# Optimization experiments

Measured on AMD Instinct MI355X. Metric: run time of the kernel, lower is better.

The kernel has to match this reference:

```python
import jax, jax.numpy as jnp
import numpy as np
from functools import partial

N_SEEDS = 1000       # n
BG_LOW, BG_UP = 0.3, 0.7
ERODE_K, ERODE_ITER = 11, 1
KSZ = 3
IGNORE = -255
INT_MAX = np.iinfo(np.int32).max


def _min_pool2d(x, k):
    # binary erosion with a kxk all-ones structuring element, SAME padding
    return jax.lax.reduce_window(x, INT_MAX, jax.lax.min, (k, k), (1, 1), 'SAME')


def _max_pool3d(x, k):
    # binary dilation over (B,H,W) with kxk window on spatial dims
    return jax.lax.reduce_window(x, -INT_MAX, jax.lax.max, (1, k, k), (1, 1, 1), 'SAME')


def _otsu_threshold(flat255):
    # flat255: int32 pixel values in [0,255]
    hist = jnp.zeros(256, jnp.float32).at[flat255].add(1.0)
    total = jnp.asarray(flat255.shape[0], jnp.float32)
    bins = jnp.arange(256, dtype=jnp.float32)
    w = jnp.cumsum(hist)                 # class-0 pixel count up to bin t
    m = jnp.cumsum(hist * bins)          # class-0 intensity mass up to t
    mT = m[-1]
    denom = w * (total - w)
    sigma_b = jnp.where(denom > 0, (mT * w - total * m) ** 2 / (denom * total * total), 0.0)
    th = jnp.argmax(sigma_b).astype(jnp.float32)
    bad = jnp.sum(hist > 0) <= 1         # degenerate histogram -> bad_egg
    return th, bad


def _sample_mask(eligible, key, hw):
    # uniform sampling without replacement of min(N_SEEDS, #eligible)
    # via random-score top-k restricted to eligible positions
    scores = jnp.where(eligible, jax.random.uniform(key, (hw,)), -jnp.inf)
    vals, idx = jax.lax.top_k(scores, N_SEEDS)
    sel = (vals > -jnp.inf).astype(jnp.int32)
    return jnp.zeros(hw, jnp.int32).at[idx].max(sel)


def _one_sample(cam, key):
    h, w = cam.shape
    hw = h * w
    cam255 = jnp.floor(cam * 255.0)
    flat255 = jnp.clip(cam255.astype(jnp.int32).ravel(), 0, 255)

    th, bad = _otsu_threshold(flat255)
    th = jnp.where(bad, jnp.median(cam * 255.0), th)
    th = jnp.where(th == 0, 1.0, jnp.where(th == 255, 254.0, th))

    roi = (cam255 > th).astype(jnp.int32)
    for _ in range(ERODE_ITER):
        roi = _min_pool2d(roi, ERODE_K)

    kf, kb, kz = jax.random.split(key, 3)
    # foreground: sample uniformly from eroded ROI pixels
    fg = _sample_mask(roi.ravel() == 1, kf, hw)
    # background: sample uniformly from the nbr_bg lowest-activation pixels
    z = jax.random.uniform(kz, (), minval=BG_LOW, maxval=BG_UP)
    nbr_bg = jnp.ceil(z * hw)
    order = jnp.argsort(cam.ravel())
    rank = jnp.zeros(hw, jnp.int32).at[order].set(jnp.arange(hw, dtype=jnp.int32))
    bg = _sample_mask(rank.astype(jnp.float32) < nbr_bg, kb, hw)
    return fg.reshape(h, w), bg.reshape(h, w)


def setup_inputs() -> dict:
    key = jax.random.key(0)
    x = jax.random.uniform(key, (128, 1, 512, 512), dtype=jnp.float32)
    return {"x": x}


def reference(x):
    b, d, h, w = x.shape
    keys = jax.random.split(jax.random.key(42), b)
    all_fg, all_bg = jax.vmap(_one_sample)(x[:, 0], keys)   # (B,H,W) int32
    # dilation with ksz x ksz ones kernel
    all_fg = _max_pool3d(all_fg, KSZ)
    all_bg = _max_pool3d(all_bg, KSZ)
    outer = all_fg + all_bg
    all_fg = jnp.where(outer == 2, 0, all_fg)
    all_bg = jnp.where(outer == 2, 0, all_bg)
    out = jnp.full((b, h, w), IGNORE, dtype=jnp.int32)
    out = jnp.where(all_fg == 1, 1, out)
    out = jnp.where(all_bg == 1, 0, out)
    return out
```

## Files before the change

### kernel.cpp

```cpp
#include <hip/hip_runtime.h>
#include <cstdint>

typedef unsigned short u16;

constexpr int BATCH = 128;
constexpr int H = 512, W = 512;
constexpr int HW = H * W;
constexpr int WPR = W / 64;
constexpr int WPI = HW / 64;
constexpr int NSEED = 1000;
constexpr int MARGIN = 3000;
constexpr int CAP2 = 4096;
constexpr int CAPS = 1024;
constexpr int LBUF = 2048;
constexpr int NBIN = 4096;
constexpr int QSEG = 128;

__device__ __forceinline__ uint32_t rotl32(uint32_t v, int d) {
  return (v << d) | (v >> (32 - d));
}

__device__ __forceinline__ void tf2x32(uint32_t k0, uint32_t k1,
                                       uint32_t x0, uint32_t x1,
                                       uint32_t &o0, uint32_t &o1) {
// ... 121 lines not shown
__global__ __launch_bounds__(256) void k_otsu(const uint32_t* __restrict__ gh,
                                              const uint32_t* __restrict__ kbg,
                                              int* __restrict__ th_out,
                                              uint32_t* __restrict__ b1a,
                                              uint32_t* __restrict__ r1a) {
  __shared__ uint32_t h[NBIN];
  __shared__ float Lc[511], Sc[511], Lm[511], Sm[511];
  __shared__ float av[4];
  __shared__ int ai[4];
  int b = blockIdx.x, t = threadIdx.x;
  const uint32_t* g0 = gh + ((size_t)(b * 4 + 0) << 12);
  const uint32_t* g1 = gh + ((size_t)(b * 4 + 1) << 12);
  const uint32_t* g2 = gh + ((size_t)(b * 4 + 2) << 12);
  const uint32_t* g3 = gh + ((size_t)(b * 4 + 3) << 12);
  for (int i = t; i < NBIN; i += 256) h[i] = g0[i] + g1[i] + g2[i] + g3[i];
  __syncthreads();
  uint32_t hv = 0;
#pragma unroll
  for (int i = 0; i < 16; ++i) hv += h[t * 16 + ((i + t) & 15)];
  Lc[t] = (float)hv;
  Lm[t] = __fmul_rn((float)hv, (float)t);
  __syncthreads();
  lds_tree_cumsum256x2(Lc, Sc, Lm, Sm, t);
  uint32_t K = kbg[b];
  {
    float total = (float)HW;
    float mT = Sm[255];
    float w = Sc[t];
    float denom = __fmul_rn(w, __fsub_rn(total, w));
    float s = 0.0f;
    if (denom > 0.0f) {
      float d  = __fsub_rn(__fmul_rn(mT, w), __fmul_rn(total, Sm[t]));
      float nu = __fmul_rn(d, d);
      float dd = __fmul_rn(__fmul_rn(denom, total), total);
      s = __fdiv_rn(nu, dd);
    }
    float bv = s; int bidx = t;
#pragma unroll
    for (int d = 32; d >= 1; d >>= 1) {
      float ov = __shfl_xor(bv, d, 64);
      int oi = __shfl_xor(bidx, d, 64);
      if (ov > bv || (ov == bv && oi < bidx)) { bv = ov; bidx = oi; }
    }
    if ((t & 63) == 0) { av[t >> 6] = bv; ai[t >> 6] = bidx; }
    bool gf = (Sc[t] >= (float)K) && (t == 0 || Sc[t - 1] < (float)K);
    if (gf) {
      uint32_t accv = (t == 0) ? 0u : (uint32_t)Sc[t - 1];
      uint32_t b1v = 0, r1v = 1;
      for (int bin = t * 16; bin < t * 16 + 16; ++bin) {
        uint32_t cc = h[bin];
        if (accv + cc >= K) { b1v = (uint32_t)bin; r1v = K - accv; break; }
        accv += cc;
      }
      b1a[b] = b1v; r1a[b] = r1v;
    }
  }
  __syncthreads();
  if (t == 0) {
    float bv = av[0]; int bidx = ai[0];
#pragma unroll
    for (int wv = 1; wv < 4; ++wv) {
      float ov = av[wv]; int oi = ai[wv];
      if (ov > bv || (ov == bv && oi < bidx)) { bv = ov; bidx = oi; }
    }
    int bi = bidx;
    if (bi == 0) bi = 1;
    if (bi == 255) bi = 254;
    th_out[b] = bi;
  }
}

__global__ __launch_bounds__(1024) void k_main(const u16* __restrict__ gq,
                                               const float* __restrict__ x,
                                               const int* __restrict__ th,
                                               const uint32_t* __restrict__ b1a,
                                               const uint32_t* __restrict__ Tbg,
                                               const uint32_t* __restrict__ keys,
                                               uint32_t* __restrict__ Efg,
                                               uint32_t* __restrict__ cnt_bg,
                                               uint64_t* __restrict__ list,
                                               uint32_t* __restrict__ cnt_be,
                                               uint64_t* __restrict__ list_be,
                                               uint64_t* __restrict__ erod) {
  __shared__ uint64_t sroi[1104];
  __shared__ uint64_t srow[1104];
  __shared__ uint64_t lbuf[LBUF];
  __shared__ uint32_t wq[16 * QSEG];
  __shared__ uint32_t lcnt, gbase;
  int b = blockIdx.x >> 2, sub = blockIdx.x & 3, t = threadIdx.x;
  int wave = t >> 6, lane = t & 63;
  int R0 = sub * 128;
  int rlo = max(R0 - 5, 0), rhi = min(R0 + 133, H);
  int nwords = (rhi - rlo) * 8;
  const u16* gb = gq + (size_t)b * HW;
  const float* xb = x + (size_t)b * HW;
  int groi = (th[b] + 1) << 4;
  uint32_t b1 = b1a[b];
  uint32_t T = Tbg[b];
  uint32_t k0 = keys[b * 4 + 2], k1 = keys[b * 4 + 3];
  if (t == 0) lcnt = 0;
  __syncthreads();
  uint32_t* q = wq + wave * QSEG;
  uint32_t qlen = 0, hd = 0;
  uint64_t lmask = (1ull << lane) - 1ull;
  for (int r = 0; r < 8; ++r) {
    int absr = R0 + wave * 8 + r;
    int rowbase = absr * W + lane;
    int swbase = (absr - rlo) * 8;
    const u16* gp8 = gb + rowbase;
    u16 gvals[8];
#pragma unroll
    for (int c = 0; c < 8; ++c) gvals[c] = gp8[c * 64];
#pragma unroll
    for (int c = 0; c < 8; ++c) {
      uint32_t gv = (uint32_t)gvals[c];
      uint64_t bw = __ballot((int)gv >= groi);
      if (lane == 0) sroi[swbase + c] = bw;
      bool elig = gv < b1;
      uint64_t m = __ballot(elig);
      if (elig) {
        uint32_t rank = (uint32_t)__popcll(m & lmask);
        uint32_t idx = hd + qlen + rank;
        if (idx >= (uint32_t)QSEG) idx -= (uint32_t)QSEG;
        q[idx] = (uint32_t)(rowbase + c * 64);
      }
      qlen += (uint32_t)__popcll(m);
      if (gv == b1) {
        uint32_t gp = atomicAdd(&cnt_be[b], 1u);
        if (gp < (uint32_t)CAPS)
          list_be[(size_t)b * CAPS + gp] =
              (((uint64_t)__float_as_uint(xb[rowbase + c * 64])) << 18) |
              (uint32_t)(rowbase + c * 64);
      }
      while (qlen >= 64u) {
        __builtin_amdgcn_wave_barrier();
        uint32_t idx = hd + (uint32_t)lane;
        if (idx >= (uint32_t)QSEG) idx -= (uint32_t)QSEG;
        uint32_t p = q[idx];
        hd += 64u; if (hd >= (uint32_t)QSEG) hd -= (uint32_t)QSEG;
        qlen -= 64u;
        uint32_t v = score_bits(k0, k1, p) >> 9;
        if (v >= T) {
          uint32_t pos = atomicAdd(&lcnt, 1u);
          uint64_t key = (((uint64_t)((~v) & 0x7FFFFFu)) << 18) | p;
          if (pos < (uint32_t)LBUF) lbuf[pos] = key;
          else { uint32_t gp = atomicAdd(&cnt_bg[b], 1u);
                 if (gp < (uint32_t)CAP2) list[(size_t)b * CAP2 + gp] = key; }
        }
      }
    }
  }
  if (qlen) {
    __builtin_amdgcn_wave_barrier();
    if ((uint32_t)lane < qlen) {
      uint32_t idx = hd + (uint32_t)lane;
      if (idx >= (uint32_t)QSEG) idx -= (uint32_t)QSEG;
      uint32_t p = q[idx];
      uint32_t v = score_bits(k0, k1, p) >> 9;
      if (v >= T) {
        uint32_t pos = atomicAdd(&lcnt, 1u);
        uint64_t key = (((uint64_t)((~v) & 0x7FFFFFu)) << 18) | p;
        if (pos < (uint32_t)LBUF) lbuf[pos] = key;
        else { uint32_t gp = atomicAdd(&cnt_bg[b], 1u);
               if (gp < (uint32_t)CAP2) list[(size_t)b * CAP2 + gp] = key; }
      }
    }
  }
  {
    int lowWords = (R0 - rlo) * 8;
    int nh = nwords - 1024;
    for (int i = wave; i < nh; i += 16) {
      int wi = i + ((i < lowWords) ? 0 : 1024);
      int absr = rlo + (wi >> 3);
      int c = wi & 7;
      uint32_t gv = (uint32_t)gb[absr * W + c * 64 + lane];
      uint64_t bw = __ballot((int)gv >= groi);
      if (lane == 0) sroi[wi] = bw;
    }
  }
  __syncthreads();
  for (int wi = t; wi < nwords; wi += 1024) {
    int c = wi & 7;
    uint64_t cur = sroi[wi];
    uint64_t left  = (c > 0) ? sroi[wi - 1] : ~0ull;
    uint64_t right = (c < 7) ? sroi[wi + 1] : ~0ull;
    uint64_t res = cur;
#pragma unroll
    for (int s = 1; s <= 5; ++s) {
      res &= (cur >> s) | (right << (64 - s));
      res &= (cur << s) | (left >> (64 - s));
    }
    srow[wi] = res;
  }
  __syncthreads();
  {
    int coreRow = t >> 3, c = t & 7;
    int absr = R0 + coreRow;
    int s = absr - rlo;
    uint64_t res = srow[s * 8 + c];
#pragma unroll
    for (int d = 1; d <= 5; ++d) {
      if (absr - d >= 0) res &= srow[(s - d) * 8 + c];
      if (absr + d < H)  res &= srow[(s + d) * 8 + c];
    }
    erod[(size_t)b * WPI + absr * 8 + c] = res;
    uint32_t pc = (uint32_t)__popcll(res);
    for (int sh = 32; sh >= 1; sh >>= 1) pc += __shfl_down(pc, sh);
    if (lane == 0 && pc) atomicAdd(&Efg[b], pc);
  }
  __syncthreads();
  int m = min((int)lcnt, LBUF);
  if (t == 0) gbase = atomicAdd(&cnt_bg[b], (uint32_t)m);
  __syncthreads();
  uint32_t base = gbase;
  for (int i = t; i < m; i += 1024) {
    uint32_t pos = base + (uint32_t)i;
    if (pos < (uint32_t)CAP2) list[(size_t)b * CAP2 + pos] = lbuf[i];
  }
}

__global__ __launch_bounds__(1024) void k_select(const uint32_t* __restrict__ r1a,
                                                 const uint32_t* __restrict__ cnt_be,
                                                 const uint64_t* __restrict__ list_be,
                                                 const uint32_t* __restrict__ Tbg,
                                                 const uint32_t* __restrict__ keys,
                                                 const uint32_t* __restrict__ cnt_bg,
                                                 const uint64_t* __restrict__ list,
                                                 uint64_t* __restrict__ bmG,
                                                 const uint32_t* __restrict__ Ea,
                                                 uint32_t* __restrict__ cnt_fg,
                                                 uint64_t* __restrict__ list_fg,
                                                 const uint64_t* __restrict__ bmE,
                                                 uint64_t* __restrict__ bmF) {
  __shared__ uint64_t pool[5248];
  __shared__ uint32_t ecnt, tcnt, lcnt, gbase, sb2, sr2;
  int t = threadIdx.x;
  uint32_t* h = (uint32_t*)(pool + 2048);
  uint64_t* tie = pool + 4096;
  uint32_t* S = (uint32_t*)(pool + 5120);
  if (blockIdx.x < BATCH) {
    int b = blockIdx.x;
    uint64_t* ks = pool;
    uint64_t* ebuf = pool + 1024;
    uint64_t* bg = bmG + (size_t)b * WPI;
    for (int i = t; i < WPI; i += 1024) bg[i] = 0;
    int nbe = min((int)cnt_be[b], CAPS);
    if (t == 0) { ecnt = 0; tcnt = 0; }
    if (t < nbe) ks[t] = list_be[(size_t)b * CAPS + t];
    __syncthreads();
    if (t < nbe) {
      uint64_t mk = ks[t];
      int rank = 0;
      for (int i = 0; i < nbe; ++i) rank += (ks[i] < mk) ? 1 : 0;
      int r = min((int)r1a[b], nbe);
      if (rank < r) {
        uint32_t p = (uint32_t)(mk & 0x3FFFFull);
        uint32_t v = score_bits(keys[b * 4 + 2], keys[b * 4 + 3], p) >> 9;
        if (v >= Tbg[b]) {
          uint32_t slot = atomicAdd(&ecnt, 1u);
          ebuf[slot] = (((uint64_t)((~v) & 0x7FFFFFu)) << 18) | p;
        }
      }
    }
    for (int i = t; i < 4096; i += 1024) h[i] = 0;
    __syncthreads();
    int n0 = min((int)cnt_bg[b], CAP2);
    int ne = (int)ecnt;
    int n = n0 + ne;
    if (n == 0) return;
    uint32_t target = (uint32_t)min(NSEED, n);
    const uint64_t* lb = list + (size_t)b * CAP2;
    uint64_t K0 = (t < n0)        ? lb[t]        : 0;
    uint64_t K1 = (t + 1024 < n0) ? lb[t + 1024] : 0;
    uint64_t K2 = (t + 2048 < n0) ? lb[t + 2048] : 0;
    uint64_t K3 = (t + 3072 < n0) ? lb[t + 3072] : 0;
    uint64_t KE = (t < ne)        ? ebuf[t]      : 0;
    if (t < n0)        atomicAdd(&h[(uint32_t)(K0 >> 29)], 1u);
    if (t + 1024 < n0) atomicAdd(&h[(uint32_t)(K1 >> 29)], 1u);
    if (t + 2048 < n0) atomicAdd(&h[(uint32_t)(K2 >> 29)], 1u);
    if (t + 3072 < n0) atomicAdd(&h[(uint32_t)(K3 >> 29)], 1u);
    if (t < ne)        atomicAdd(&h[(uint32_t)(KE >> 29)], 1u);
    __syncthreads();
    if (t < 256) {
      uint32_t s = 0;
#pragma unroll
      for (int i = 0; i < 16; ++i) s += h[t * 16 + ((i + t) & 15)];
      S[t] = s;
    }
    __syncthreads();
    for (int st = 1; st < 256; st <<= 1) {
      uint32_t v = 0;
      if (t < 256 && t >= st) v = S[t - st];
      __syncthreads();
      if (t < 256) S[t] += v;
      __syncthreads();
    }
    if (t < 256) {
      uint32_t before = (t == 0) ? 0u : S[t - 1];
      if (S[t] >= target && before < target) {
        uint32_t acc = before;
        for (int i = 0; i < 16; ++i) {
          uint32_t c = h[t * 16 + i];
          if (acc + c >= target) { sb2 = (uint32_t)(t * 16 + i); sr2 = target - acc; break; }
          acc += c;
        }
      }
    }
    __syncthreads();
    uint32_t b2 = sb2, r2 = sr2;
#define PROC(KK, VALID) \
    if (VALID) { \
      uint32_t bin = (uint32_t)((KK) >> 29); \
      if (bin < b2) { \
        uint32_t p = (uint32_t)(KK) & 0x3FFFFu; \
        atomicOr((unsigned long long*)&bg[p >> 6], 1ull << (p & 63)); \
      } else if (bin == b2) { \
        uint32_t pos = atomicAdd(&tcnt, 1u); \
        if (pos < 1024u) tie[pos] = (KK); \
      } \
    }
    PROC(K0, t < n0) PROC(K1, t + 1024 < n0) PROC(K2, t + 2048 < n0)
    PROC(K3, t + 3072 < n0) PROC(KE, t < ne)
#undef PROC
    __syncthreads();
    int m = min((int)tcnt, 1024);
    int r = min((int)r2, m);
    if (t < m) {
      uint64_t mk = tie[t];
      int rank = 0;
      for (int i = 0; i < m; ++i) rank += (tie[i] < mk) ? 1 : 0;
      if (rank < r) {
        uint32_t p = (uint32_t)mk & 0x3FFFFu;
        atomicOr((unsigned long long*)&bg[p >> 6], 1ull << (p & 63));
      }
    }
  } else {
    int b = blockIdx.x - BATCH;
    uint32_t E = Ea[b];
    if (E <= (uint32_t)NSEED) return;
    uint64_t* lbuf = pool;
    const uint64_t* eb = bmE + (size_t)b * WPI;
    uint64_t* ob = bmF + (size_t)b * WPI;
    for (int i = t; i < WPI; i += 1024) ob[i] = 0;
    if (t == 0) { lcnt = 0; tcnt = 0; }
    __syncthreads();
    float tvf = floorf((1.0f - (float)MARGIN / (float)E) * 8388608.0f);
    uint32_t T = (uint32_t)fmaxf(tvf, 0.0f);
    uint32_t k0 = keys[b * 4 + 0], k1 = keys[b * 4 + 1];
    int lane = t & 63;
    for (int k = 0; k < HW / 1024; ++k) {
      uint32_t p = (uint32_t)(k * 1024 + t);
      uint64_t wbits = eb[p >> 6];
      if ((wbits >> lane) & 1ull) {
        uint32_t v = score_bits(k0, k1, p) >> 9;
        if (v >= T) {
          uint32_t pos = atomicAdd(&lcnt, 1u);
          uint64_t key = (((uint64_t)((~v) & 0x7FFFFFu)) << 18) | p;
          if (pos < (uint32_t)LBUF) lbuf[pos] = key;
          else { uint32_t gp = atomicAdd(&cnt_fg[b], 1u);
                 if (gp < (uint32_t)CAP2) list_fg[(size_t)b * CAP2 + gp] = key; }
        }
      }
    }
    __syncthreads();
    int m2 = min((int)lcnt, LBUF);
    if (t == 0) gbase = atomicAdd(&cnt_fg[b], (uint32_t)m2);
    __syncthreads();
    for (int i = t; i < m2; i += 1024) {
      uint32_t pos = gbase + (uint32_t)i;
      if (pos < (uint32_t)CAP2) list_fg[(size_t)b * CAP2 + pos] = lbuf[i];
    }
    __syncthreads();
    int n = min((int)cnt_fg[b], CAP2);
    if (n == 0) return;
    uint32_t target = (uint32_t)min(NSEED, n);
    const uint64_t* lb = list_fg + (size_t)b * CAP2;
    uint64_t K0 = (t < n)        ? lb[t]        : 0;
    uint64_t K1 = (t + 1024 < n) ? lb[t + 1024] : 0;
    uint64_t K2 = (t + 2048 < n) ? lb[t + 2048] : 0;
    uint64_t K3 = (t + 3072 < n) ? lb[t + 3072] : 0;
    for (int i = t; i < 4096; i += 1024) h[i] = 0;
    __syncthreads();
    if (t < n)        atomicAdd(&h[(uint32_t)(K0 >> 29)], 1u);
    if (t + 1024 < n) atomicAdd(&h[(uint32_t)(K1 >> 29)], 1u);
    if (t + 2048 < n) atomicAdd(&h[(uint32_t)(K2 >> 29)], 1u);
    if (t + 3072 < n) atomicAdd(&h[(uint32_t)(K3 >> 29)], 1u);
    __syncthreads();
    if (t < 256) {
      uint32_t s = 0;
#pragma unroll
      for (int i = 0; i < 16; ++i) s += h[t * 16 + ((i + t) & 15)];
      S[t] = s;
    }
    __syncthreads();
    for (int st = 1; st < 256; st <<= 1) {
      uint32_t v = 0;
      if (t < 256 && t >= st) v = S[t - st];
      __syncthreads();
      if (t < 256) S[t] += v;
      __syncthreads();
    }
    if (t < 256) {
      uint32_t before = (t == 0) ? 0u : S[t - 1];
      if (S[t] >= target && before < target) {
        uint32_t acc = before;
        for (int i = 0; i < 16; ++i) {
          uint32_t c = h[t * 16 + i];
          if (acc + c >= target) { sb2 = (uint32_t)(t * 16 + i); sr2 = target - acc; break; }
          acc += c;
        }
      }
    }
    __syncthreads();
    uint32_t b2 = sb2, r2 = sr2;
#define PROC(KK, VALID) \
    if (VALID) { \
      uint32_t bin = (uint32_t)((KK) >> 29); \
      if (bin < b2) { \
        uint32_t p = (uint32_t)(KK) & 0x3FFFFu; \
        atomicOr((unsigned long long*)&ob[p >> 6], 1ull << (p & 63)); \
      } else if (bin == b2) { \
        uint32_t pos = atomicAdd(&tcnt, 1u); \
        if (pos < 1024u) tie[pos] = (KK); \
      } \
    }
    PROC(K0, t < n) PROC(K1, t + 1024 < n) PROC(K2, t + 2048 < n) PROC(K3, t + 3072 < n)
#undef PROC
    __syncthreads();
    int m = min((int)tcnt, 1024);
    int r = min((int)r2, m);
    if (t < m) {
      uint64_t mk = tie[t];
      int rank = 0;
      for (int i = 0; i < m; ++i) rank += (tie[i] < mk) ? 1 : 0;
      if (rank < r) {
        uint32_t p = (uint32_t)mk & 0x3FFFFu;
        atomicOr((unsigned long long*)&ob[p >> 6], 1ull << (p & 63));
      }
    }
  }
}

__global__ __launch_bounds__(256) void k_compose2(const uint64_t* __restrict__ bmE,
                                                  const uint64_t* __restrict__ bmF,
                                                  const uint64_t* __restrict__ G,
                                                  const uint32_t* __restrict__ Ea,
                                                  int* __restrict__ out) {
  __shared__ uint64_t FdS[64], BdS[64];
  int blk = blockIdx.x;
  int b = blk >> 6, rg = blk & 63;
  int t = threadIdx.x;
  const uint64_t* Fsrc = (Ea[b] <= (uint32_t)NSEED) ? bmE : bmF;
  const uint64_t* Fb = Fsrc + (size_t)b * WPI;
  const uint64_t* Gb = G + (size_t)b * WPI;
  if (t < 128) {
    const uint64_t* src = (t < 64) ? Fb : Gb;
    int w = t & 63;
    int r = rg * 8 + (w >> 3), c = w & 7;
    uint64_t d = 0;
#pragma unroll
    for (int dr = -1; dr <= 1; ++dr) {
      int rr = r + dr;
      if (rr < 0 || rr >= H) continue;
      int wi = rr * 8 + c;
      uint64_t cur = src[wi];
      uint64_t lf = (c > 0) ? src[wi - 1] : 0ull;
      uint64_t rt = (c < 7) ? src[wi + 1] : 0ull;
      d |= cur | (cur << 1) | (lf >> 63) | (cur >> 1) | (rt << 63);
    }
    if (t < 64) FdS[w] = d; else BdS[w] = d;
  }
  __syncthreads();
  int4* ob = (int4*)out + ((size_t)b * HW + (size_t)rg * 4096) / 4;
  for (int i = t; i < 1024; i += 256) {
    int w = i >> 4, sub = i & 15;
    uint64_t Fd = FdS[w], Bd = BdS[w];
    uint64_t ov = Fd & Bd;
    Fd &= ~ov; Bd &= ~ov;
    int sh = sub * 4;
    int4 o;
    o.x = ((Fd >> (sh + 0)) & 1ull) ? 1 : (((Bd >> (sh + 0)) & 1ull) ? 0 : -255);
    o.y = ((Fd >> (sh + 1)) & 1ull) ? 1 : (((Bd >> (sh + 1)) & 1ull) ? 0 : -255);
    o.z = ((Fd >> (sh + 2)) & 1ull) ? 1 : (((Bd >> (sh + 2)) & 1ull) ? 0 : -255);
    o.w = ((Fd >> (sh + 3)) & 1ull) ? 1 : (((Bd >> (sh + 3)) & 1ull) ? 0 : -255);
    ob[i] = o;
  }
}

extern "C" void kernel_launch(void* const* d_in, const int* in_sizes, int n_in,
                              void* d_out, int out_size, void* d_ws, size_t ws_size,
                              hipStream_t stream) {
  (void)in_sizes; (void)n_in; (void)out_size; (void)ws_size;
  const float* x = (const float*)d_in[0];
  int* out = (int*)d_out;
  char* ws = (char*)d_ws;

  u16* g = (u16*)d_out;

  uint32_t* keys   = (uint32_t*)(ws + 0);
  uint32_t* kbg    = (uint32_t*)(ws + 2048);
  int*      th     = (int*)     (ws + 2560);
  uint32_t* b1a    = (uint32_t*)(ws + 3072);
  uint32_t* r1a    = (uint32_t*)(ws + 3584);
  uint32_t* Tbg    = (uint32_t*)(ws + 4096);
  uint32_t* Efg    = (uint32_t*)(ws + 4608);
  uint32_t* cnt_fg = (uint32_t*)(ws + 5120);
  uint32_t* cnt_be = (uint32_t*)(ws + 5632);
  uint32_t* cnt_bg = (uint32_t*)(ws + 6144);
  uint32_t* gh      = (uint32_t*)(ws + 8192);
  uint64_t* bmG     = (uint64_t*)(ws + 8192 + 8388608);
  uint64_t* list    = (uint64_t*)(ws + 8192 + 8388608 + 4194304);
  uint64_t* list_be = (uint64_t*)(ws + 8192 + 8388608 + 8388608);
  uint64_t* bmE     = (uint64_t*)(ws + 8192 + 8388608 + 9437184);
  uint64_t* bmF     = (uint64_t*)(ws + 8192 + 8388608 + 13631488);
  uint64_t* list_fg = (uint64_t*)gh;

  k_binify   <<<BATCH * 4, 1024, 0, stream>>>((const float4*)x, g, gh, keys, kbg,
                                              Tbg, Efg, cnt_fg, cnt_be, cnt_bg);
  k_otsu     <<<BATCH, 256, 0, stream>>>(gh, kbg, th, b1a, r1a);
  k_main     <<<BATCH * 4, 1024, 0, stream>>>(g, x, th, b1a, Tbg, keys,
                                              Efg, cnt_bg, list, cnt_be, list_be, bmE);
  k_select   <<<BATCH * 2, 1024, 0, stream>>>(r1a, cnt_be, list_be, Tbg, keys,
                                              cnt_bg, list, bmG,
                                              Efg, cnt_fg, list_fg, bmE, bmF);
  k_compose2 <<<BATCH * 64, 256, 0, stream>>>(bmE, bmF, bmG, Efg, out);
}
```

Baseline: 343.0 us.

## Split k_main into separate erosion and background-sampling block roles

```diff
diff --git a/kernel.cpp b/kernel.cpp
--- a/kernel.cpp
+++ b/kernel.cpp
@@ -227,140 +227,137 @@
                                                uint32_t* __restrict__ cnt_be,
                                                uint64_t* __restrict__ list_be,
                                                uint64_t* __restrict__ erod) {
-  __shared__ uint64_t sroi[1104];
-  __shared__ uint64_t srow[1104];
-  __shared__ uint64_t lbuf[LBUF];
-  __shared__ uint32_t wq[16 * QSEG];
+  __shared__ union {
+    struct { uint64_t sroi[1104]; uint64_t srow[1104]; } e;
+    struct { uint32_t wq[16 * QSEG]; uint64_t lbuf[LBUF]; } s;
+  } u;
   __shared__ uint32_t lcnt, gbase;
-  int b = blockIdx.x >> 2, sub = blockIdx.x & 3, t = threadIdx.x;
+  int b = blockIdx.x >> 3, role = blockIdx.x & 7, t = threadIdx.x;
   int wave = t >> 6, lane = t & 63;
-  int R0 = sub * 128;
-  int rlo = max(R0 - 5, 0), rhi = min(R0 + 133, H);
-  int nwords = (rhi - rlo) * 8;
   const u16* gb = gq + (size_t)b * HW;
-  const float* xb = x + (size_t)b * HW;
-  int groi = (th[b] + 1) << 4;
-  uint32_t b1 = b1a[b];
-  uint32_t T = Tbg[b];
-  uint32_t k0 = keys[b * 4 + 2], k1 = keys[b * 4 + 3];
-  if (t == 0) lcnt = 0;
-  __syncthreads();
-  uint32_t* q = wq + wave * QSEG;
-  uint32_t qlen = 0, hd = 0;
-  uint64_t lmask = (1ull << lane) - 1ull;
-  for (int r = 0; r < 8; ++r) {
-    int absr = R0 + wave * 8 + r;
-    int rowbase = absr * W + lane;
-    int swbase = (absr - rlo) * 8;
-    const u16* gp8 = gb + rowbase;
-    u16 gvals[8];
-#pragma unroll
-    for (int c = 0; c < 8; ++c) gvals[c] = gp8[c * 64];
-#pragma unroll
-    for (int c = 0; c < 8; ++c) {
-      uint32_t gv = (uint32_t)gvals[c];
+
+  if (role < 4) {
+    int sub = role;
+    int R0 = sub * 128;
+    int rlo = max(R0 - 5, 0), rhi = min(R0 + 133, H);
+    int nwords = (rhi - rlo) * 8;
+    int groi = (th[b] + 1) << 4;
+    for (int wi = wave; wi < nwords; wi += 16) {
+      int absr = rlo + (wi >> 3), c = wi & 7;
+      uint32_t gv = (uint32_t)gb[absr * W + c * 64 + lane];
       uint64_t bw = __ballot((int)gv >= groi);
-      if (lane == 0) sroi[swbase + c] = bw;
-      bool elig = gv < b1;
-      uint64_t m = __ballot(elig);
-      if (elig) {
-        uint32_t rank = (uint32_t)__popcll(m & lmask);
-        uint32_t idx = hd + qlen + rank;
-        if (idx >= (uint32_t)QSEG) idx -= (uint32_t)QSEG;
-        q[idx] = (uint32_t)(rowbase + c * 64);
-      }
-      qlen += (uint32_t)__popcll(m);
-      if (gv == b1) {
-        uint32_t gp = atomicAdd(&cnt_be[b], 1u);
-        if (gp < (uint32_t)CAPS)
-          list_be[(size_t)b * CAPS + gp] =
-              (((uint64_t)__float_as_uint(xb[rowbase + c * 64])) << 18) |
-              (uint32_t)(rowbase + c * 64);
-      }
-      while (qlen >= 64u) {
-        __builtin_amdgcn_wave_barrier();
+      if (lane == 0) u.e.sroi[wi] = bw;
+    }
+    __syncthreads();
+    for (int wi = t; wi < nwords; wi += 1024) {
+      int c = wi & 7;
+      uint64_t cur = u.e.sroi[wi];
+      uint64_t left  = (c > 0) ? u.e.sroi[wi - 1] : ~0ull;
+      uint64_t right = (c < 7) ? u.e.sroi[wi + 1] : ~0ull;
+      uint64_t res = cur;
+#pragma unroll
+      for (int s = 1; s <= 5; ++s) {
+        res &= (cur >> s) | (right << (64 - s));
+        res &= (cur << s) | (left >> (64 - s));
+      }
+      u.e.srow[wi] = res;
+    }
+    __syncthreads();
+    {
+      int coreRow = t >> 3, c = t & 7;
+      int absr = R0 + coreRow;
+      int s = absr - rlo;
+      uint64_t res = u.e.srow[s * 8 + c];
+#pragma unroll
+      for (int d = 1; d <= 5; ++d) {
+        if (absr - d >= 0) res &= u.e.srow[(s - d) * 8 + c];
+        if (absr + d < H)  res &= u.e.srow[(s + d) * 8 + c];
+      }
+      erod[(size_t)b * WPI + absr * 8 + c] = res;
+      uint32_t pc = (uint32_t)__popcll(res);
+      for (int sh = 32; sh >= 1; sh >>= 1) pc += __shfl_down(pc, sh);
+      if (lane == 0 && pc) atomicAdd(&Efg[b], pc);
+    }
+  } else {
+    int q = role - 4;
+    uint32_t b1 = b1a[b];
+    uint32_t T = Tbg[b];
+    uint32_t k0 = keys[b * 4 + 2], k1 = keys[b * 4 + 3];
+    const float* xb = x + (size_t)b * HW;
+    if (t == 0) lcnt = 0;
+    __syncthreads();
+    uint32_t* ring = u.s.wq + wave * QSEG;
+    uint32_t qlen = 0, hd = 0;
+    uint64_t lmask = (1ull << lane) - 1ull;
+    uint32_t pbase = (uint32_t)(q * (HW / 4));
+    const ushort4* g4 = (const ushort4*)(gb + pbase);
+    for (int it = 0; it < (HW / 4) / 4096; ++it) {
+      int i = it * 1024 + t;
+      ushort4 gv4 = g4[i];
+      uint32_t p0 = pbase + (uint32_t)i * 4u;
+      uint32_t gs[4] = {gv4.x, gv4.y, gv4.z, gv4.w};
+#pragma unroll
+      for (int j = 0; j < 4; ++j) {
+        uint32_t gv = gs[j];
+        bool elig = gv < b1;
+        uint64_t m = __ballot(elig);
+        if (elig) {
+          uint32_t rank = (uint32_t)__popcll(m & lmask);
+          uint32_t idx = hd + qlen + rank;
+          if (idx >= (uint32_t)QSEG) idx -= (uint32_t)QSEG;
+          ring[idx] = p0 + (uint32_t)j;
+        }
+        qlen += (uint32_t)__popcll(m);
+        if (gv == b1) {
+          uint32_t gp = atomicAdd(&cnt_be[b], 1u);
+          if (gp < (uint32_t)CAPS)
+            list_be[(size_t)b * CAPS + gp] =
+                (((uint64_t)__float_as_uint(xb[p0 + j])) << 18) |
+                (uint32_t)(p0 + j);
+        }
+        while (qlen >= 64u) {
+          __builtin_amdgcn_wave_barrier();
+          uint32_t idx = hd + (uint32_t)lane;
+          if (idx >= (uint32_t)QSEG) idx -= (uint32_t)QSEG;
+          uint32_t p = ring[idx];
+          hd += 64u; if (hd >= (uint32_t)QSEG) hd -= (uint32_t)QSEG;
+          qlen -= 64u;
+          uint32_t v = score_bits(k0, k1, p) >> 9;
+          if (v >= T) {
+            uint32_t pos = atomicAdd(&lcnt, 1u);
+            uint64_t key = (((uint64_t)((~v) & 0x7FFFFFu)) << 18) | p;
+            if (pos < (uint32_t)LBUF) u.s.lbuf[pos] = key;
+            else { uint32_t gp = atomicAdd(&cnt_bg[b], 1u);
+                   if (gp < (uint32_t)CAP2) list[(size_t)b * CAP2 + gp] = key; }
+          }
+        }
+      }
+    }
+    if (qlen) {
+      __builtin_amdgcn_wave_barrier();
+      if ((uint32_t)lane < qlen) {
         uint32_t idx = hd + (uint32_t)lane;
         if (idx >= (uint32_t)QSEG) idx -= (uint32_t)QSEG;
-        uint32_t p = q[idx];
-        hd += 64u; if (hd >= (uint32_t)QSEG) hd -= (uint32_t)QSEG;
-        qlen -= 64u;
+        uint32_t p = ring[idx];
         uint32_t v = score_bits(k0, k1, p) >> 9;
         if (v >= T) {
           uint32_t pos = atomicAdd(&lcnt, 1u);
           uint64_t key = (((uint64_t)((~v) & 0x7FFFFFu)) << 18) | p;
-          if (pos < (uint32_t)LBUF) lbuf[pos] = key;
+          if (pos < (uint32_t)LBUF) u.s.lbuf[pos] = key;
           else { uint32_t gp = atomicAdd(&cnt_bg[b], 1u);
                  if (gp < (uint32_t)CAP2) list[(size_t)b * CAP2 + gp] = key; }
         }
       }
     }
-  }
-  if (qlen) {
-    __builtin_amdgcn_wave_barrier();
-    if ((uint32_t)lane < qlen) {
-      uint32_t idx = hd + (uint32_t)lane;
-      if (idx >= (uint32_t)QSEG) idx -= (uint32_t)QSEG;
-      uint32_t p = q[idx];
-      uint32_t v = score_bits(k0, k1, p) >> 9;
-      if (v >= T) {
-        uint32_t pos = atomicAdd(&lcnt, 1u);
-        uint64_t key = (((uint64_t)((~v) & 0x7FFFFFu)) << 18) | p;
-        if (pos < (uint32_t)LBUF) lbuf[pos] = key;
-        else { uint32_t gp = atomicAdd(&cnt_bg[b], 1u);
-               if (gp < (uint32_t)CAP2) list[(size_t)b * CAP2 + gp] = key; }
-      }
-    }
-  }
-  {
-    int lowWords = (R0 - rlo) * 8;
-    int nh = nwords - 1024;
-    for (int i = wave; i < nh; i += 16) {
-      int wi = i + ((i < lowWords) ? 0 : 1024);
-      int absr = rlo + (wi >> 3);
-      int c = wi & 7;
-      uint32_t gv = (uint32_t)gb[absr * W + c * 64 + lane];
-      uint64_t bw = __ballot((int)gv >= groi);
-      if (lane == 0) sroi[wi] = bw;
-    }
-  }
-  __syncthreads();
-  for (int wi = t; wi < nwords; wi += 1024) {
-    int c = wi & 7;
-    uint64_t cur = sroi[wi];
-    uint64_t left  = (c > 0) ? sroi[wi - 1] : ~0ull;
-    uint64_t right = (c < 7) ? sroi[wi + 1] : ~0ull;
-    uint64_t res = cur;
-#pragma unroll
-    for (int s = 1; s <= 5; ++s) {
-      res &= (cur >> s) | (right << (64 - s));
-      res &= (cur << s) | (left >> (64 - s));
-    }
-    srow[wi] = res;
-  }
-  __syncthreads();
-  {
-    int coreRow = t >> 3, c = t & 7;
-    int absr = R0 + coreRow;
-    int s = absr - rlo;
-    uint64_t res = srow[s * 8 + c];
-#pragma unroll
-    for (int d = 1; d <= 5; ++d) {
-      if (absr - d >= 0) res &= srow[(s - d) * 8 + c];
-      if (absr + d < H)  res &= srow[(s + d) * 8 + c];
-    }
-    erod[(size_t)b * WPI + absr * 8 + c] = res;
-    uint32_t pc = (uint32_t)__popcll(res);
-    for (int sh = 32; sh >= 1; sh >>= 1) pc += __shfl_down(pc, sh);
-    if (lane == 0 && pc) atomicAdd(&Efg[b], pc);
-  }
-  __syncthreads();
-  int m = min((int)lcnt, LBUF);
-  if (t == 0) gbase = atomicAdd(&cnt_bg[b], (uint32_t)m);
-  __syncthreads();
-  uint32_t base = gbase;
-  for (int i = t; i < m; i += 1024) {
-    uint32_t pos = base + (uint32_t)i;
-    if (pos < (uint32_t)CAP2) list[(size_t)b * CAP2 + pos] = lbuf[i];
+    __syncthreads();
+    int m = min((int)lcnt, LBUF);
+    if (t == 0) gbase = atomicAdd(&cnt_bg[b], (uint32_t)m);
+    __syncthreads();
+    uint32_t base = gbase;
+    for (int i = t; i < m; i += 1024) {
+      uint32_t pos = base + (uint32_t)i;
+      if (pos < (uint32_t)CAP2) list[(size_t)b * CAP2 + pos] = u.s.lbuf[i];
+    }
   }
 }
 
@@ -663,7 +660,7 @@
   k_binify   <<<BATCH * 4, 1024, 0, stream>>>((const float4*)x, g, gh, keys, kbg,
                                               Tbg, Efg, cnt_fg, cnt_be, cnt_bg);
   k_otsu     <<<BATCH, 256, 0, stream>>>(gh, kbg, th, b1a, r1a);
-  k_main     <<<BATCH * 4, 1024, 0, stream>>>(g, x, th, b1a, Tbg, keys,
+  k_main     <<<BATCH * 8, 1024, 0, stream>>>(g, x, th, b1a, Tbg, keys,
                                               Efg, cnt_bg, list, cnt_be, list_be, bmE);
   k_select   <<<BATCH * 2, 1024, 0, stream>>>(r1a, cnt_be, list_be, Tbg, keys,
                                               cnt_bg, list, bmG,
```

Result: slower. 384.8 us (+12.2%).

## Fuse seed selection and output composition into one kernel with LDS bitmaps

Applied to the files above, without the earlier changes.

```diff
diff --git a/kernel.cpp b/kernel.cpp
--- a/kernel.cpp
+++ b/kernel.cpp
@@ -364,33 +364,35 @@
   }
 }
 
-__global__ __launch_bounds__(1024) void k_select(const uint32_t* __restrict__ r1a,
-                                                 const uint32_t* __restrict__ cnt_be,
-                                                 const uint64_t* __restrict__ list_be,
-                                                 const uint32_t* __restrict__ Tbg,
-                                                 const uint32_t* __restrict__ keys,
-                                                 const uint32_t* __restrict__ cnt_bg,
-                                                 const uint64_t* __restrict__ list,
-                                                 uint64_t* __restrict__ bmG,
-                                                 const uint32_t* __restrict__ Ea,
-                                                 uint32_t* __restrict__ cnt_fg,
-                                                 uint64_t* __restrict__ list_fg,
-                                                 const uint64_t* __restrict__ bmE,
-                                                 uint64_t* __restrict__ bmF) {
+__global__ __launch_bounds__(1024) void k_selcomp(const uint32_t* __restrict__ r1a,
+                                                  const uint32_t* __restrict__ cnt_be,
+                                                  const uint64_t* __restrict__ list_be,
+                                                  const uint32_t* __restrict__ Tbg,
+                                                  const uint32_t* __restrict__ keys,
+                                                  const uint32_t* __restrict__ cnt_bg,
+                                                  const uint64_t* __restrict__ list,
+                                                  const uint32_t* __restrict__ Ea,
+                                                  uint32_t* __restrict__ cnt_fg,
+                                                  uint64_t* __restrict__ list_fg,
+                                                  const uint64_t* __restrict__ bmE,
+                                                  int* __restrict__ out) {
+  __shared__ uint64_t Gbit[WPI];
+  __shared__ uint64_t Fbit[WPI];
   __shared__ uint64_t pool[5248];
   __shared__ uint32_t ecnt, tcnt, lcnt, gbase, sb2, sr2;
-  int t = threadIdx.x;
+  int b = blockIdx.x, t = threadIdx.x;
+  uint32_t* G32 = (uint32_t*)Gbit;
+  uint32_t* F32 = (uint32_t*)Fbit;
   uint32_t* h = (uint32_t*)(pool + 2048);
   uint64_t* tie = pool + 4096;
   uint32_t* S = (uint32_t*)(pool + 5120);
-  if (blockIdx.x < BATCH) {
-    int b = blockIdx.x;
+  for (int i = t; i < WPI; i += 1024) { Gbit[i] = 0; Fbit[i] = 0; }
+  if (t == 0) { ecnt = 0; tcnt = 0; }
+
+  {
     uint64_t* ks = pool;
     uint64_t* ebuf = pool + 1024;
-    uint64_t* bg = bmG + (size_t)b * WPI;
-    for (int i = t; i < WPI; i += 1024) bg[i] = 0;
     int nbe = min((int)cnt_be[b], CAPS);
-    if (t == 0) { ecnt = 0; tcnt = 0; }
     if (t < nbe) ks[t] = list_be[(size_t)b * CAPS + t];
     __syncthreads();
     if (t < nbe) {
@@ -412,223 +414,228 @@
     int n0 = min((int)cnt_bg[b], CAP2);
     int ne = (int)ecnt;
     int n = n0 + ne;
-    if (n == 0) return;
-    uint32_t target = (uint32_t)min(NSEED, n);
-    const uint64_t* lb = list + (size_t)b * CAP2;
-    uint64_t K0 = (t < n0)        ? lb[t]        : 0;
-    uint64_t K1 = (t + 1024 < n0) ? lb[t + 1024] : 0;
-    uint64_t K2 = (t + 2048 < n0) ? lb[t + 2048] : 0;
-    uint64_t K3 = (t + 3072 < n0) ? lb[t + 3072] : 0;
-    uint64_t KE = (t < ne)        ? ebuf[t]      : 0;
-    if (t < n0)        atomicAdd(&h[(uint32_t)(K0 >> 29)], 1u);
-    if (t + 1024 < n0) atomicAdd(&h[(uint32_t)(K1 >> 29)], 1u);
-    if (t + 2048 < n0) atomicAdd(&h[(uint32_t)(K2 >> 29)], 1u);
-    if (t + 3072 < n0) atomicAdd(&h[(uint32_t)(K3 >> 29)], 1u);
-    if (t < ne)        atomicAdd(&h[(uint32_t)(KE >> 29)], 1u);
+    if (n > 0) {
+      uint32_t target = (uint32_t)min(NSEED, n);
+      const uint64_t* lb = list + (size_t)b * CAP2;
+      uint64_t K0 = (t < n0)        ? lb[t]        : 0;
+      uint64_t K1 = (t + 1024 < n0) ? lb[t + 1024] : 0;
+      uint64_t K2 = (t + 2048 < n0) ? lb[t + 2048] : 0;
+      uint64_t K3 = (t + 3072 < n0) ? lb[t + 3072] : 0;
+      uint64_t KE = (t < ne)        ? ebuf[t]      : 0;
+      if (t < n0)        atomicAdd(&h[(uint32_t)(K0 >> 29)], 1u);
+      if (t + 1024 < n0) atomicAdd(&h[(uint32_t)(K1 >> 29)], 1u);
+      if (t + 2048 < n0) atomicAdd(&h[(uint32_t)(K2 >> 29)], 1u);
+      if (t + 3072 < n0) atomicAdd(&h[(uint32_t)(K3 >> 29)], 1u);
+      if (t < ne)        atomicAdd(&h[(uint32_t)(KE >> 29)], 1u);
+      __syncthreads();
+      if (t < 256) {
+        uint32_t s = 0;
+#pragma unroll
+        for (int i = 0; i < 16; ++i) s += h[t * 16 + ((i + t) & 15)];
+        S[t] = s;
+      }
+      __syncthreads();
+      for (int st = 1; st < 256; st <<= 1) {
+        uint32_t v = 0;
+        if (t < 256 && t >= st) v = S[t - st];
+        __syncthreads();
+        if (t < 256) S[t] += v;
+        __syncthreads();
+      }
+      if (t < 256) {
+        uint32_t before = (t == 0) ? 0u : S[t - 1];
+        if (S[t] >= target && before < target) {
+          uint32_t acc = before;
+          for (int i = 0; i < 16; ++i) {
+            uint32_t c = h[t * 16 + i];
+            if (acc + c >= target) { sb2 = (uint32_t)(t * 16 + i); sr2 = target - acc; break; }
+            acc += c;
+          }
+        }
+      }
+      __syncthreads();
+      uint32_t b2 = sb2, r2 = sr2;
+#define PROCB(KK, VALID) \
+      if (VALID) { \
+        uint32_t bin = (uint32_t)((KK) >> 29); \
+        if (bin < b2) { \
+          uint32_t p = (uint32_t)(KK) & 0x3FFFFu; \
+          atomicOr(&G32[p >> 5], 1u << (p & 31)); \
+        } else if (bin == b2) { \
+          uint32_t pos = atomicAdd(&tcnt, 1u); \
+          if (pos < 1024u) tie[pos] = (KK); \
+        } \
+      }
+      PROCB(K0, t < n0) PROCB(K1, t + 1024 < n0) PROCB(K2, t + 2048 < n0)
+      PROCB(K3, t + 3072 < n0) PROCB(KE, t < ne)
+#undef PROCB
+      __syncthreads();
+      int m = min((int)tcnt, 1024);
+      int r = min((int)r2, m);
+      if (t < m) {
+        uint64_t mk = tie[t];
+        int rank = 0;
+        for (int i = 0; i < m; ++i) rank += (tie[i] < mk) ? 1 : 0;
+        if (rank < r) {
+          uint32_t p = (uint32_t)mk & 0x3FFFFu;
+          atomicOr(&G32[p >> 5], 1u << (p & 31));
+        }
+      }
+    }
+  }
+  __syncthreads();
+
+  {
+    uint32_t E = Ea[b];
+    const uint64_t* eb = bmE + (size_t)b * WPI;
+    if (E <= (uint32_t)NSEED) {
+      for (int i = t; i < WPI; i += 1024) Fbit[i] = eb[i];
+      __syncthreads();
+    } else {
+      uint64_t* lbuf = pool;
+      if (t == 0) { lcnt = 0; tcnt = 0; }
+      for (int i = t; i < 4096; i += 1024) h[i] = 0;
+      __syncthreads();
+      float tvf = floorf((1.0f - (float)MARGIN / (float)E) * 8388608.0f);
+      uint32_t T = (uint32_t)fmaxf(tvf, 0.0f);
+      uint32_t k0 = keys[b * 4 + 0], k1 = keys[b * 4 + 1];
+      int lane = t & 63;
+      for (int k = 0; k < HW / 1024; ++k) {
+        uint32_t p = (uint32_t)(k * 1024 + t);
+        uint64_t wbits = eb[p >> 6];
+        if ((wbits >> lane) & 1ull) {
+          uint32_t v = score_bits(k0, k1, p) >> 9;
+          if (v >= T) {
+            uint32_t pos = atomicAdd(&lcnt, 1u);
+            uint64_t key = (((uint64_t)((~v) & 0x7FFFFFu)) << 18) | p;
+            if (pos < (uint32_t)LBUF) lbuf[pos] = key;
+            else { uint32_t gp = atomicAdd(&cnt_fg[b], 1u);
+                   if (gp < (uint32_t)CAP2) list_fg[(size_t)b * CAP2 + gp] = key; }
+          }
+        }
+      }
+      __syncthreads();
+      int m2 = min((int)lcnt, LBUF);
+      if (t == 0) gbase = atomicAdd(&cnt_fg[b], (uint32_t)m2);
+      __syncthreads();
+      for (int i = t; i < m2; i += 1024) {
+        uint32_t pos = gbase + (uint32_t)i;
+        if (pos < (uint32_t)CAP2) list_fg[(size_t)b * CAP2 + pos] = lbuf[i];
+      }
+      __syncthreads();
+      int n = min((int)cnt_fg[b], CAP2);
+      if (n > 0) {
+        uint32_t target = (uint32_t)min(NSEED, n);
+        const uint64_t* lb = list_fg + (size_t)b * CAP2;
+        uint64_t K0 = (t < n)        ? lb[t]        : 0;
+        uint64_t K1 = (t + 1024 < n) ? lb[t + 1024] : 0;
+        uint64_t K2 = (t + 2048 < n) ? lb[t + 2048] : 0;
+        uint64_t K3 = (t + 3072 < n) ? lb[t + 3072] : 0;
+        if (t < n)        atomicAdd(&h[(uint32_t)(K0 >> 29)], 1u);
+        if (t + 1024 < n) atomicAdd(&h[(uint32_t)(K1 >> 29)], 1u);
+        if (t + 2048 < n) atomicAdd(&h[(uint32_t)(K2 >> 29)], 1u);
+        if (t + 3072 < n) atomicAdd(&h[(uint32_t)(K3 >> 29)], 1u);
+        __syncthreads();
+        if (t < 256) {
+          uint32_t s = 0;
+#pragma unroll
+          for (int i = 0; i < 16; ++i) s += h[t * 16 + ((i + t) & 15)];
+          S[t] = s;
+        }
+        __syncthreads();
+        for (int st = 1; st < 256; st <<= 1) {
+          uint32_t v = 0;
+          if (t < 256 && t >= st) v = S[t - st];
+          __syncthreads();
+          if (t < 256) S[t] += v;
+          __syncthreads();
+        }
+        if (t < 256) {
+          uint32_t before = (t == 0) ? 0u : S[t - 1];
+          if (S[t] >= target && before < target) {
+            uint32_t acc = before;
+            for (int i = 0; i < 16; ++i) {
+              uint32_t c = h[t * 16 + i];
+              if (acc + c >= target) { sb2 = (uint32_t)(t * 16 + i); sr2 = target - acc; break; }
+              acc += c;
+            }
+          }
+        }
+        __syncthreads();
+        uint32_t b2 = sb2, r2 = sr2;
+#define PROCF(KK, VALID) \
+        if (VALID) { \
+          uint32_t bin = (uint32_t)((KK) >> 29); \
+          if (bin < b2) { \
+            uint32_t p = (uint32_t)(KK) & 0x3FFFFu; \
+            atomicOr(&F32[p >> 5], 1u << (p & 31)); \
+          } else if (bin == b2) { \
+            uint32_t pos = atomicAdd(&tcnt, 1u); \
+            if (pos < 1024u) tie[pos] = (KK); \
+          } \
+        }
+        PROCF(K0, t < n) PROCF(K1, t + 1024 < n) PROCF(K2, t + 2048 < n)
+        PROCF(K3, t + 3072 < n)
+#undef PROCF
+        __syncthreads();
+        int m = min((int)tcnt, 1024);
+        int r = min((int)r2, m);
+        if (t < m) {
+          uint64_t mk = tie[t];
+          int rank = 0;
+          for (int i = 0; i < m; ++i) rank += (tie[i] < mk) ? 1 : 0;
+          if (rank < r) {
+            uint32_t p = (uint32_t)mk & 0x3FFFFu;
+            atomicOr(&F32[p >> 5], 1u << (p & 31));
+          }
+        }
+      }
+      __syncthreads();
+    }
+  }
+  __syncthreads();
+
+  uint64_t* FdS = pool;
+  uint64_t* BdS = pool + 512;
+  for (int it = 0; it < 8; ++it) {
+    {
+      int s = t >> 7, xx = t & 127;
+      int w = xx & 63;
+      int rg = it * 8 + s;
+      int r = rg * 8 + (w >> 3), c = w & 7;
+      const uint64_t* src = (xx < 64) ? Fbit : Gbit;
+      uint64_t d = 0;
+#pragma unroll
+      for (int dr = -1; dr <= 1; ++dr) {
+        int rr = r + dr;
+        if (rr < 0 || rr >= H) continue;
+        int wi = rr * 8 + c;
+        uint64_t cur = src[wi];
+        uint64_t lf = (c > 0) ? src[wi - 1] : 0ull;
+        uint64_t rt = (c < 7) ? src[wi + 1] : 0ull;
+        d |= cur | (cur << 1) | (lf >> 63) | (cur >> 1) | (rt << 63);
+      }
+      if (xx < 64) FdS[s * 64 + w] = d; else BdS[s * 64 + w] = d;
+    }
     __syncthreads();
-    if (t < 256) {
-      uint32_t s = 0;
-#pragma unroll
-      for (int i = 0; i < 16; ++i) s += h[t * 16 + ((i + t) & 15)];
-      S[t] = s;
+    int4* ob = (int4*)out + (size_t)b * (HW / 4) + (size_t)it * 8192;
+#pragma unroll
+    for (int k2 = 0; k2 < 8; ++k2) {
+      int idx = k2 * 1024 + t;
+      int ss = idx >> 10, i = idx & 1023;
+      int ww = i >> 4, sub = i & 15;
+      uint64_t Fd = FdS[ss * 64 + ww], Bd = BdS[ss * 64 + ww];
+      uint64_t ov = Fd & Bd;
+      Fd &= ~ov; Bd &= ~ov;
+      int sh = sub * 4;
+      int4 o;
+      o.x = ((Fd >> (sh + 0)) & 1ull) ? 1 : (((Bd >> (sh + 0)) & 1ull) ? 0 : -255);
+      o.y = ((Fd >> (sh + 1)) & 1ull) ? 1 : (((Bd >> (sh + 1)) & 1ull) ? 0 : -255);
+      o.z = ((Fd >> (sh + 2)) & 1ull) ? 1 : (((Bd >> (sh + 2)) & 1ull) ? 0 : -255);
+      o.w = ((Fd >> (sh + 3)) & 1ull) ? 1 : (((Bd >> (sh + 3)) & 1ull) ? 0 : -255);
+      ob[idx] = o;
     }
     __syncthreads();
-    for (int st = 1; st < 256; st <<= 1) {
-      uint32_t v = 0;
-      if (t < 256 && t >= st) v = S[t - st];
-      __syncthreads();
-      if (t < 256) S[t] += v;
-      __syncthreads();
-    }
-    if (t < 256) {
-      uint32_t before = (t == 0) ? 0u : S[t - 1];
-      if (S[t] >= target && before < target) {
-        uint32_t acc = before;
-        for (int i = 0; i < 16; ++i) {
-          uint32_t c = h[t * 16 + i];
-          if (acc + c >= target) { sb2 = (uint32_t)(t * 16 + i); sr2 = target - acc; break; }
-          acc += c;
-        }
-      }
-    }
-    __syncthreads();
-    uint32_t b2 = sb2, r2 = sr2;
-#define PROC(KK, VALID) \
-    if (VALID) { \
-      uint32_t bin = (uint32_t)((KK) >> 29); \
-      if (bin < b2) { \
-        uint32_t p = (uint32_t)(KK) & 0x3FFFFu; \
-        atomicOr((unsigned long long*)&bg[p >> 6], 1ull << (p & 63)); \
-      } else if (bin == b2) { \
-        uint32_t pos = atomicAdd(&tcnt, 1u); \
-        if (pos < 1024u) tie[pos] = (KK); \
-      } \
-    }
-    PROC(K0, t < n0) PROC(K1, t + 1024 < n0) PROC(K2, t + 2048 < n0)
-    PROC(K3, t + 3072 < n0) PROC(KE, t < ne)
-#undef PROC
-    __syncthreads();
-    int m = min((int)tcnt, 1024);
-    int r = min((int)r2, m);
-    if (t < m) {
-      uint64_t mk = tie[t];
-      int rank = 0;
-      for (int i = 0; i < m; ++i) rank += (tie[i] < mk) ? 1 : 0;
-      if (rank < r) {
-        uint32_t p = (uint32_t)mk & 0x3FFFFu;
-        atomicOr((unsigned long long*)&bg[p >> 6], 1ull << (p & 63));
-      }
-    }
-  } else {
-    int b = blockIdx.x - BATCH;
-    uint32_t E = Ea[b];
-    if (E <= (uint32_t)NSEED) return;
-    uint64_t* lbuf = pool;
-    const uint64_t* eb = bmE + (size_t)b * WPI;
-    uint64_t* ob = bmF + (size_t)b * WPI;
-    for (int i = t; i < WPI; i += 1024) ob[i] = 0;
-    if (t == 0) { lcnt = 0; tcnt = 0; }
-    __syncthreads();
-    float tvf = floorf((1.0f - (float)MARGIN / (float)E) * 8388608.0f);
-    uint32_t T = (uint32_t)fmaxf(tvf, 0.0f);
-    uint32_t k0 = keys[b * 4 + 0], k1 = keys[b * 4 + 1];
-    int lane = t & 63;
-    for (int k = 0; k < HW / 1024; ++k) {
-      uint32_t p = (uint32_t)(k * 1024 + t);
-      uint64_t wbits = eb[p >> 6];
-      if ((wbits >> lane) & 1ull) {
-        uint32_t v = score_bits(k0, k1, p) >> 9;
-        if (v >= T) {
-          uint32_t pos = atomicAdd(&lcnt, 1u);
-          uint64_t key = (((uint64_t)((~v) & 0x7FFFFFu)) << 18) | p;
-          if (pos < (uint32_t)LBUF) lbuf[pos] = key;
-          else { uint32_t gp = atomicAdd(&cnt_fg[b], 1u);
-                 if (gp < (uint32_t)CAP2) list_fg[(size_t)b * CAP2 + gp] = key; }
-        }
-      }
-    }
-    __syncthreads();
-    int m2 = min((int)lcnt, LBUF);
-    if (t == 0) gbase = atomicAdd(&cnt_fg[b], (uint32_t)m2);
-    __syncthreads();
-    for (int i = t; i < m2; i += 1024) {
-      uint32_t pos = gbase + (uint32_t)i;
-      if (pos < (uint32_t)CAP2) list_fg[(size_t)b * CAP2 + pos] = lbuf[i];
-    }
-    __syncthreads();
-    int n = min((int)cnt_fg[b], CAP2);
-    if (n == 0) return;
-    uint32_t target = (uint32_t)min(NSEED, n);
-    const uint64_t* lb = list_fg + (size_t)b * CAP2;
-    uint64_t K0 = (t < n)        ? lb[t]        : 0;
-    uint64_t K1 = (t + 1024 < n) ? lb[t + 1024] : 0;
-    uint64_t K2 = (t + 2048 < n) ? lb[t + 2048] : 0;
-    uint64_t K3 = (t + 3072 < n) ? lb[t + 3072] : 0;
-    for (int i = t; i < 4096; i += 1024) h[i] = 0;
-    __syncthreads();
-    if (t < n)        atomicAdd(&h[(uint32_t)(K0 >> 29)], 1u);
-    if (t + 1024 < n) atomicAdd(&h[(uint32_t)(K1 >> 29)], 1u);
-    if (t + 2048 < n) atomicAdd(&h[(uint32_t)(K2 >> 29)], 1u);
-    if (t + 3072 < n) atomicAdd(&h[(uint32_t)(K3 >> 29)], 1u);
-    __syncthreads();
-    if (t < 256) {
-      uint32_t s = 0;
-#pragma unroll
-      for (int i = 0; i < 16; ++i) s += h[t * 16 + ((i + t) & 15)];
-      S[t] = s;
-    }
-    __syncthreads();
-    for (int st = 1; st < 256; st <<= 1) {
-      uint32_t v = 0;
-      if (t < 256 && t >= st) v = S[t - st];
-      __syncthreads();
-      if (t < 256) S[t] += v;
-      __syncthreads();
-    }
-    if (t < 256) {
-      uint32_t before = (t == 0) ? 0u : S[t - 1];
-      if (S[t] >= target && before < target) {
-        uint32_t acc = before;
-        for (int i = 0; i < 16; ++i) {
-          uint32_t c = h[t * 16 + i];
-          if (acc + c >= target) { sb2 = (uint32_t)(t * 16 + i); sr2 = target - acc; break; }
-          acc += c;
-        }
-      }
-    }
-    __syncthreads();
-    uint32_t b2 = sb2, r2 = sr2;
-#define PROC(KK, VALID) \
-    if (VALID) { \
-      uint32_t bin = (uint32_t)((KK) >> 29); \
-      if (bin < b2) { \
-        uint32_t p = (uint32_t)(KK) & 0x3FFFFu; \
-        atomicOr((unsigned long long*)&ob[p >> 6], 1ull << (p & 63)); \
-      } else if (bin == b2) { \
-        uint32_t pos = atomicAdd(&tcnt, 1u); \
-        if (pos < 1024u) tie[pos] = (KK); \
-      } \
-    }
-    PROC(K0, t < n) PROC(K1, t + 1024 < n) PROC(K2, t + 2048 < n) PROC(K3, t + 3072 < n)
-#undef PROC
-    __syncthreads();
-    int m = min((int)tcnt, 1024);
-    int r = min((int)r2, m);
-    if (t < m) {
-      uint64_t mk = tie[t];
-      int rank = 0;
-      for (int i = 0; i < m; ++i) rank += (tie[i] < mk) ? 1 : 0;
-      if (rank < r) {
-        uint32_t p = (uint32_t)mk & 0x3FFFFu;
-        atomicOr((unsigned long long*)&ob[p >> 6], 1ull << (p & 63));
-      }
-    }
-  }
-}
-
-__global__ __launch_bounds__(256) void k_compose2(const uint64_t* __restrict__ bmE,
-                                                  const uint64_t* __restrict__ bmF,
-                                                  const uint64_t* __restrict__ G,
-                                                  const uint32_t* __restrict__ Ea,
-                                                  int* __restrict__ out) {
-  __shared__ uint64_t FdS[64], BdS[64];
-  int blk = blockIdx.x;
-  int b = blk >> 6, rg = blk & 63;
-  int t = threadIdx.x;
-  const uint64_t* Fsrc = (Ea[b] <= (uint32_t)NSEED) ? bmE : bmF;
-  const uint64_t* Fb = Fsrc + (size_t)b * WPI;
-  const uint64_t* Gb = G + (size_t)b * WPI;
-  if (t < 128) {
-    const uint64_t* src = (t < 64) ? Fb : Gb;
-    int w = t & 63;
-    int r = rg * 8 + (w >> 3), c = w & 7;
-    uint64_t d = 0;
-#pragma unroll
-    for (int dr = -1; dr <= 1; ++dr) {
-      int rr = r + dr;
-      if (rr < 0 || rr >= H) continue;
-      int wi = rr * 8 + c;
-      uint64_t cur = src[wi];
-      uint64_t lf = (c > 0) ? src[wi - 1] : 0ull;
-      uint64_t rt = (c < 7) ? src[wi + 1] : 0ull;
-      d |= cur | (cur << 1) | (lf >> 63) | (cur >> 1) | (rt << 63);
-    }
-    if (t < 64) FdS[w] = d; else BdS[w] = d;
-  }
-  __syncthreads();
-  int4* ob = (int4*)out + ((size_t)b * HW + (size_t)rg * 4096) / 4;
-  for (int i = t; i < 1024; i += 256) {
-    int w = i >> 4, sub = i & 15;
-    uint64_t Fd = FdS[w], Bd = BdS[w];
-    uint64_t ov = Fd & Bd;
-    Fd &= ~ov; Bd &= ~ov;
-    int sh = sub * 4;
-    int4 o;
-    o.x = ((Fd >> (sh + 0)) & 1ull) ? 1 : (((Bd >> (sh + 0)) & 1ull) ? 0 : -255);
-    o.y = ((Fd >> (sh + 1)) & 1ull) ? 1 : (((Bd >> (sh + 1)) & 1ull) ? 0 : -255);
-    o.z = ((Fd >> (sh + 2)) & 1ull) ? 1 : (((Bd >> (sh + 2)) & 1ull) ? 0 : -255);
-    o.w = ((Fd >> (sh + 3)) & 1ull) ? 1 : (((Bd >> (sh + 3)) & 1ull) ? 0 : -255);
-    ob[i] = o;
   }
 }
 
@@ -653,20 +660,17 @@
   uint32_t* cnt_be = (uint32_t*)(ws + 5632);
   uint32_t* cnt_bg = (uint32_t*)(ws + 6144);
   uint32_t* gh      = (uint32_t*)(ws + 8192);
-  uint64_t* bmG     = (uint64_t*)(ws + 8192 + 8388608);
-  uint64_t* list    = (uint64_t*)(ws + 8192 + 8388608 + 4194304);
-  uint64_t* list_be = (uint64_t*)(ws + 8192 + 8388608 + 8388608);
-  uint64_t* bmE     = (uint64_t*)(ws + 8192 + 8388608 + 9437184);
-  uint64_t* bmF     = (uint64_t*)(ws + 8192 + 8388608 + 13631488);
+  uint64_t* list    = (uint64_t*)(ws + 8192 + 8388608);
+  uint64_t* list_be = (uint64_t*)(ws + 8192 + 8388608 + 4194304);
+  uint64_t* bmE     = (uint64_t*)(ws + 8192 + 8388608 + 5242880);
   uint64_t* list_fg = (uint64_t*)gh;
 
-  k_binify   <<<BATCH * 4, 1024, 0, stream>>>((const float4*)x, g, gh, keys, kbg,
-                                              Tbg, Efg, cnt_fg, cnt_be, cnt_bg);
-  k_otsu     <<<BATCH, 256, 0, stream>>>(gh, kbg, th, b1a, r1a);
-  k_main     <<<BATCH * 4, 1024, 0, stream>>>(g, x, th, b1a, Tbg, keys,
-                                              Efg, cnt_bg, list, cnt_be, list_be, bmE);
-  k_select   <<<BATCH * 2, 1024, 0, stream>>>(r1a, cnt_be, list_be, Tbg, keys,
-                                              cnt_bg, list, bmG,
-                                              Efg, cnt_fg, list_fg, bmE, bmF);
-  k_compose2 <<<BATCH * 64, 256, 0, stream>>>(bmE, bmF, bmG, Efg, out);
-}
+  k_binify  <<<BATCH * 4, 1024, 0, stream>>>((const float4*)x, g, gh, keys, kbg,
+                                             Tbg, Efg, cnt_fg, cnt_be, cnt_bg);
+  k_otsu    <<<BATCH, 256, 0, stream>>>(gh, kbg, th, b1a, r1a);
+  k_main    <<<BATCH * 4, 1024, 0, stream>>>(g, x, th, b1a, Tbg, keys,
+                                             Efg, cnt_bg, list, cnt_be, list_be, bmE);
+  k_selcomp <<<BATCH, 1024, 0, stream>>>(r1a, cnt_be, list_be, Tbg, keys,
+                                         cnt_bg, list, Efg, cnt_fg, list_fg,
+                                         bmE, out);
+}
```

Result: no change. 339.3 us (-1.1%).
